# Optimization experiments

Hardware: AMD Instinct MI355X
Metric: run time of the kernel (lower is better)

The kernel has to match this reference:

```python
import jax, jax.numpy as jnp
import numpy as np

DIM = 1024
INNER = DIM // 2
DSTATE = 8
KSZ = 3
DTRANK = max(INNER // 8, 4)
B, L = 4, 4096


def setup_inputs() -> dict:
    key = jax.random.key(0)
    ks = jax.random.split(key, 8)
    s = 0.02
    x = jax.random.normal(ks[0], (B, L, DIM), dtype=jnp.float32)
    W_in = jax.random.normal(ks[1], (DIM, DIM), dtype=jnp.float32) * s
    Kx = jax.random.normal(ks[2], (INNER, 1, KSZ), dtype=jnp.float32) * 0.1
    Kz = jax.random.normal(ks[3], (INNER, 1, KSZ), dtype=jnp.float32) * 0.1
    W_xproj = jax.random.normal(ks[4], (DTRANK + 2 * DSTATE, INNER), dtype=jnp.float32) * s
    W_dt = jax.random.normal(ks[5], (INNER, DTRANK), dtype=jnp.float32) * s
    # dt bias: inverse_softplus of exp(linspace(log dt_min, log dt_max))
    dt_init = jnp.exp(jnp.linspace(jnp.log(0.02), jnp.log(0.2), INNER))
    b_dt = jnp.log(jnp.expm1(dt_init)).astype(jnp.float32)
    A_log = jnp.log(jnp.tile(jnp.arange(1, DSTATE + 1, dtype=jnp.float32), (INNER, 1)))
    D = jnp.ones((INNER,), dtype=jnp.float32)
    W_out = jax.random.normal(ks[6], (DIM, DIM), dtype=jnp.float32) * s
    return {"x": x, "W_in": W_in, "Kx": Kx, "Kz": Kz, "W_xproj": W_xproj,
            "W_dt": W_dt, "b_dt": b_dt, "A_log": A_log, "D": D, "W_out": W_out}


def _dwconv_silu(u, kern):
    # u: [B,L,C], kern: [C,1,K] depthwise (groups=C), 'same' padding
    c = u.shape[-1]
    v = jnp.transpose(u, (0, 2, 1))  # [B,C,L]
    v = jax.lax.conv_general_dilated(v, kern, (1,), [(KSZ // 2, KSZ // 2)],
                                     dimension_numbers=("NCH", "OIH", "NCH"),
                                     feature_group_count=c)
    return jax.nn.silu(jnp.transpose(v, (0, 2, 1)))


def _forward(x, W_in, Kx, Kz, W_xproj, W_dt, b_dt, A_log, D, W_out):
    h = jnp.einsum("bld,ed->ble", x, W_in)  # Linear(dim,dim), no bias
    xb, zb = jnp.split(h, 2, axis=-1)       # [B,L,INNER] each
    xb = _dwconv_silu(xb, Kx)
    zb = _dwconv_silu(zb, Kz)
    proj = jnp.einsum("blc,oc->blo", xb, W_xproj)
    dt_raw = proj[..., :DTRANK]
    b_raw = proj[..., DTRANK:DTRANK + DSTATE]
    c_raw = proj[..., DTRANK + DSTATE:]
    delta = jnp.clip(jax.nn.softplus(jnp.einsum("blr,cr->blc", dt_raw, W_dt) + b_dt), 1e-4, 1.0)  # [B,L,C]
    b_term = jnp.tanh(b_raw)  # [B,L,N]
    c_term = jnp.tanh(c_raw)  # [B,L,N]
    a = jax.nn.softplus(A_log) + 1e-4  # [C,N]
    decay = jnp.clip(jnp.exp(-delta[..., None] * a), 1e-4, 1.0)        # [B,L,C,N]
    drive = (1.0 - decay) * (b_term[:, :, None, :] * xb[..., None])    # [B,L,C,N]

    def step(state, inp):
        dec_t, drv_t, c_t, x_t = inp  # [B,C,N], [B,C,N], [B,N], [B,C]
        state = dec_t * state + drv_t
        y = jnp.sum(state * c_t[:, None, :], axis=-1) + D * x_t  # [B,C]
        return state, y

    tm = lambda t: jnp.moveaxis(t, 1, 0)  # time-major
    state0 = jnp.zeros((x.shape[0], INNER, DSTATE), dtype=jnp.float32)
    _, ys = jax.lax.scan(step, state0, (tm(decay), tm(drive), tm(c_term), tm(xb)))
    y = jnp.moveaxis(ys, 0, 1)  # [B,L,INNER]
    return jnp.einsum("bld,ed->ble", jnp.concatenate([y, zb], axis=-1), W_out)


def reference(x, W_in, Kx, Kz, W_xproj, W_dt, b_dt, A_log, D, W_out):
    return _forward(x, W_in, Kx, Kz, W_xproj, W_dt, b_dt, A_log, D, W_out)
```

## Files before the change

kernel.cpp:

```cpp
#include <hip/hip_runtime.h>


using bf16x8 = __attribute__((ext_vector_type(8))) short;
using f32x4  = __attribute__((ext_vector_type(4))) float;

__device__ __forceinline__ unsigned short f2bf(float f) {
  unsigned int u = __float_as_uint(f);
  u = u + 0x7fffu + ((u >> 16) & 1u);
  return (unsigned short)(u >> 16);
}

__device__ __forceinline__ float fsoftplus(float x) {
  return (x > 15.f) ? x : __logf(1.f + __expf(x));
}

__device__ __forceinline__ float ftanh(float x) {
  float v = fminf(fmaxf(x, -15.f), 15.f);
  float e = __expf(2.f * v);
  return (e - 1.f) / (e + 1.f);
}

__device__ __forceinline__ void cvt4(const float* __restrict__ in,
                                     unsigned short* __restrict__ out, int i) {
  float4 v = ((const float4*)in)[i];
  ushort4 o;
  o.x = f2bf(v.x); o.y = f2bf(v.y); o.z = f2bf(v.z); o.w = f2bf(v.w);
  ((ushort4*)out)[i] = o;
}

__global__ __launch_bounds__(256) void prep_all(
    const float* __restrict__ x, const float* __restrict__ Win,
    const float* __restrict__ Wout, const float* __restrict__ Wdt,
    const float* __restrict__ Wxp,
    unsigned short* __restrict__ xbf, unsigned short* __restrict__ winbf,
    unsigned short* __restrict__ woutbf, unsigned short* __restrict__ wdbf,
    unsigned short* __restrict__ wxpbf) {
  int b = blockIdx.x, t = threadIdx.x;
  if (b < 16384)      cvt4(x,    xbf,    b * 256 + t);
  else if (b < 17408) cvt4(Win,  winbf,  (b - 16384) * 256 + t);
  else if (b < 18432) cvt4(Wout, woutbf, (b - 17408) * 256 + t);
  else if (b < 18464) cvt4(Wdt,  wdbf,   (b - 18432) * 256 + t);
  else {
    int i = (b - 18464) * 256 + t;
    int row = i >> 9;
    wxpbf[i] = (row < 80) ? f2bf(Wxp[i]) : (unsigned short)0;
  }
}


__global__ __launch_bounds__(256) void gemm_proj128(
    const unsigned short* __restrict__ A,
    const unsigned short* __restrict__ B,
    unsigned short* __restrict__ dtr, float* __restrict__ bterm,
    float* __restrict__ cterm, int M, int N, int K) {
  __shared__ short As[128 * 32];
  __shared__ short Bs[128 * 32];
  const int m0 = blockIdx.x * 128;
  const int lane = threadIdx.x & 63;
  const int wv = threadIdx.x >> 6;
  const int wm = (wv >> 1) * 64;
  const int wn = (wv & 1) * 64;
  f32x4 acc[4][4] = {};
  const int row_a = wv * 32 + (lane >> 2);
  const int koff = (lane & 3) * 8;
  const unsigned short* gA = A + (size_t)(m0 + row_a) * K + koff;
  const unsigned short* gB = B + (size_t)row_a * K + koff;
  short* lA = &As[(wv * 32) * 32];
  short* lB = &Bs[(wv * 32) * 32];
  const int r = lane & 15;
  const int q = lane >> 4;
  for (int k0 = 0; k0 < K; k0 += 32) {
    __syncthreads();
    __builtin_amdgcn_global_load_lds((const __attribute__((address_space(1))) void*)(const void*)gA,
                                     (__attribute__((address_space(3))) void*)(void*)lA, 16, 0, 0);
    __builtin_amdgcn_global_load_lds((const __attribute__((address_space(1))) void*)(const void*)(gA + 16 * K),
                                     (__attribute__((address_space(3))) void*)(void*)(lA + 16 * 32), 16, 0, 0);
    __builtin_amdgcn_global_load_lds((const __attribute__((address_space(1))) void*)(const void*)gB,
                                     (__attribute__((address_space(3))) void*)(void*)lB, 16, 0, 0);
    __builtin_amdgcn_global_load_lds((const __attribute__((address_space(1))) void*)(const void*)(gB + 16 * K),
                                     (__attribute__((address_space(3))) void*)(void*)(lB + 16 * 32), 16, 0, 0);
    gA += 32; gB += 32;
    __syncthreads();
    bf16x8 av[4], bv[4];
#pragma unroll
    for (int i = 0; i < 4; ++i)
      av[i] = *(const bf16x8*)&As[(wm + i * 16 + r) * 32 + q * 8];
#pragma unroll
    for (int j = 0; j < 4; ++j)
      bv[j] = *(const bf16x8*)&Bs[(wn + j * 16 + r) * 32 + q * 8];
#pragma unroll
    for (int i = 0; i < 4; ++i)
#pragma unroll
      for (int j = 0; j < 4; ++j)
        acc[i][j] = __builtin_amdgcn_mfma_f32_16x16x32_bf16(av[i], bv[j], acc[i][j], 0, 0, 0);
  }
#pragma unroll
  for (int i = 0; i < 4; ++i)
#pragma unroll
    for (int j = 0; j < 4; ++j) {
      const int col = wn + j * 16 + r;
#pragma unroll
      for (int t = 0; t < 4; ++t) {
        const int row = m0 + wm + i * 16 + q * 4 + t;
        float v = acc[i][j][t];
        if (col < 64)      dtr[(size_t)row * 64 + col] = f2bf(v);
        else if (col < 72) bterm[(size_t)row * 8 + (col - 64)] = ftanh(v);
        else if (col < 80) cterm[(size_t)row * 8 + (col - 72)] = ftanh(v);
      }
    }
}

__global__ __launch_bounds__(256) void gemm_dt128(
    const unsigned short* __restrict__ A,
    const unsigned short* __restrict__ B,
    const float* __restrict__ bdt,
    float* __restrict__ C, int M, int N, int K) {
  __shared__ short As[128 * 32];
  __shared__ short Bs[128 * 32];
  const int m0 = blockIdx.x * 128;
  const int n0 = blockIdx.y * 128;
  const int lane = threadIdx.x & 63;
  const int wv = threadIdx.x >> 6;
  const int wm = (wv >> 1) * 64;
  const int wn = (wv & 1) * 64;
  f32x4 acc[4][4] = {};
  const int row_a = wv * 32 + (lane >> 2);
  const int koff = (lane & 3) * 8;
  const unsigned short* gA = A + (size_t)(m0 + row_a) * K + koff;
  const unsigned short* gB = B + (size_t)(n0 + row_a) * K + koff;
  short* lA = &As[(wv * 32) * 32];
  short* lB = &Bs[(wv * 32) * 32];
  const int r = lane & 15;
  const int q = lane >> 4;
  for (int k0 = 0; k0 < K; k0 += 32) {
    __syncthreads();
    __builtin_amdgcn_global_load_lds((const __attribute__((address_space(1))) void*)(const void*)gA,
                                     (__attribute__((address_space(3))) void*)(void*)lA, 16, 0, 0);
    __builtin_amdgcn_global_load_lds((const __attribute__((address_space(1))) void*)(const void*)(gA + 16 * K),
                                     (__attribute__((address_space(3))) void*)(void*)(lA + 16 * 32), 16, 0, 0);
    __builtin_amdgcn_global_load_lds((const __attribute__((address_space(1))) void*)(const void*)gB,
                                     (__attribute__((address_space(3))) void*)(void*)lB, 16, 0, 0);
    __builtin_amdgcn_global_load_lds((const __attribute__((address_space(1))) void*)(const void*)(gB + 16 * K),
                                     (__attribute__((address_space(3))) void*)(void*)(lB + 16 * 32), 16, 0, 0);
    gA += 32; gB += 32;
    __syncthreads();
    bf16x8 av[4], bv[4];
#pragma unroll
    for (int i = 0; i < 4; ++i)
      av[i] = *(const bf16x8*)&As[(wm + i * 16 + r) * 32 + q * 8];
#pragma unroll
    for (int j = 0; j < 4; ++j)
      bv[j] = *(const bf16x8*)&Bs[(wn + j * 16 + r) * 32 + q * 8];
#pragma unroll
    for (int i = 0; i < 4; ++i)
#pragma unroll
      for (int j = 0; j < 4; ++j)
        acc[i][j] = __builtin_amdgcn_mfma_f32_16x16x32_bf16(av[i], bv[j], acc[i][j], 0, 0, 0);
  }
#pragma unroll
  for (int j = 0; j < 4; ++j) {
    const int col = n0 + wn + j * 16 + r;
    const float bb = bdt[col];
#pragma unroll
    for (int i = 0; i < 4; ++i)
#pragma unroll
      for (int t = 0; t < 4; ++t) {
        float v = acc[i][j][t] + bb;
        float delta = fminf(fmaxf(fsoftplus(v), 1e-4f), 1.f);
        C[(size_t)(m0 + wm + i * 16 + q * 4 + t) * N + col] = delta;
      }
  }
}

__device__ __forceinline__ void g256_stage(short* lds, int slot,
    const unsigned short* sp, int ktIdx, int wvLds, int K) {
  const unsigned short* s = sp + ktIdx * 64;
  __builtin_amdgcn_global_load_lds((const __attribute__((address_space(1))) void*)s,
      (__attribute__((address_space(3))) void*)(lds + slot * 8192 + wvLds), 16, 0, 0);
  __builtin_amdgcn_global_load_lds((const __attribute__((address_space(1))) void*)(s + (size_t)64 * K),
      (__attribute__((address_space(3))) void*)(lds + slot * 8192 + 4096 + wvLds), 16, 0, 0);
}

template <int PAR, int MH, int NHLO, bool RA, bool RB, int SSLOT, bool VM, bool HINT>
__device__ __forceinline__ void g256_phase(
    short* lds, int aSlotOff, int bSlotOff, int aoff, int boff, int wvLds,
    bf16x8 (&av)[4][2], bf16x8 (&bv)[4][2], f32x4 (&acc)[8][4],
    const unsigned short* sp, int ktIdx, int K) {
  if (RA) {
#pragma unroll
    for (int ii = 0; ii < 4; ++ii) {
      av[ii][0] = *(const bf16x8*)&lds[PAR * 4 * 8192 + aSlotOff + MH * 4096 + ii * 1024 + aoff];
      av[ii][1] = *(const bf16x8*)&lds[PAR * 4 * 8192 + aSlotOff + MH * 4096 + ii * 1024 + (aoff ^ 32)];
    }
  }
  if (RB) {
#pragma unroll
    for (int jj = 0; jj < 2; ++jj) {
      bv[NHLO + jj][0] = *(const bf16x8*)&lds[(PAR * 4 + 2) * 8192 + bSlotOff + (NHLO + jj) * 1024 + boff];
      bv[NHLO + jj][1] = *(const bf16x8*)&lds[(PAR * 4 + 2) * 8192 + bSlotOff + (NHLO + jj) * 1024 + (boff ^ 32)];
    }
  }
  g256_stage(lds, SSLOT, sp, ktIdx, wvLds, K);
  if (HINT) asm volatile("s_waitcnt lgkmcnt(8)");
  if (VM) asm volatile("s_waitcnt vmcnt(4)" ::: "memory");
  __builtin_amdgcn_s_barrier();
  asm volatile("s_waitcnt lgkmcnt(0)" ::: "memory");
  __builtin_amdgcn_s_setprio(1);
#pragma unroll
  for (int ii = 0; ii < 4; ++ii)
#pragma unroll
    for (int jj = 0; jj < 2; ++jj) {
      acc[MH * 4 + ii][NHLO + jj] = __builtin_amdgcn_mfma_f32_16x16x32_bf16(
          av[ii][0], bv[NHLO + jj][0], acc[MH * 4 + ii][NHLO + jj], 0, 0, 0);
      acc[MH * 4 + ii][NHLO + jj] = __builtin_amdgcn_mfma_f32_16x16x32_bf16(
          av[ii][1], bv[NHLO + jj][1], acc[MH * 4 + ii][NHLO + jj], 0, 0, 0);
    }
  __builtin_amdgcn_s_setprio(0);
  __builtin_amdgcn_s_barrier();
}

__global__ __launch_bounds__(512, 2) void gemm256_bt(
    const unsigned short* __restrict__ A,
    const unsigned short* __restrict__ B,
    float* __restrict__ C, int M, int N, int K) {
  __shared__ short lds[8 * 8192];
  const int nmt = M >> 8;
  const int bid = blockIdx.x;
  const int g = nmt >> 3;
  const int xcd = bid & 7;
  const int loc = bid >> 3;
  const int mtile = xcd * g + (loc % g);
  const int ntile = loc / g;
  const int m0 = mtile << 8, n0 = ntile << 8;
  const int tid = threadIdx.x;
  const int w = tid >> 6, lane = tid & 63;
  const int r = lane & 15, q = lane >> 4;
  const int wrow = w >> 2, wcol = w & 3;
  const int srow = tid >> 3;
  const int scol = ((tid & 7) ^ (srow & 7)) << 3;
  const unsigned short* pA0 = A + (size_t)(m0 + srow) * K + scol;
  const unsigned short* pA1 = A + (size_t)(m0 + 128 + srow) * K + scol;
  const unsigned short* pB0 = B + (size_t)(n0 + srow) * K + scol;
  const unsigned short* pB1 = B + (size_t)(n0 + 128 + srow) * K + scol;
  const int wvLds = w * 512;
  const int aSlotOff = wrow * 8192;
  const int bSlotOff = (wcol >> 1) * 8192;
  const int swzc = (q * 8) ^ ((r & 7) << 3);
  const int aoff = r * 64 + swzc;
  const int boff = (wcol & 1) * 4096 + r * 64 + swzc;
  bf16x8 av[4][2], bv[4][2];
  f32x4 acc[8][4] = {};
  const int NT = K >> 6;
  const int NI = NT >> 1;
  g256_stage(lds, 0, pA0, 0, wvLds, K);
  g256_stage(lds, 1, pA1, 0, wvLds, K);
  g256_stage(lds, 2, pB0, 0, wvLds, K);
  g256_stage(lds, 3, pB1, 0, wvLds, K);
  g256_stage(lds, 6, pB0, 1, wvLds, K);
  g256_stage(lds, 7, pB1, 1, wvLds, K);
  asm volatile("s_waitcnt vmcnt(4)" ::: "memory");
  __builtin_amdgcn_s_barrier();
#pragma unroll 1
  for (int it = 0; it < NI; ++it) {
    const int ktO  = 2 * it + 1;
    const int ktE2 = (2 * it + 2 < NT) ? 2 * it + 2 : NT - 1;
    const int ktO2 = (2 * it + 3 < NT) ? 2 * it + 3 : NT - 1;
    g256_phase<0, 0, 0, true,  true,  4, false, true >(lds, aSlotOff, bSlotOff, aoff, boff, wvLds, av, bv, acc, pA0, ktO,  K);
    g256_phase<0, 0, 2, false, true,  5, false, false>(lds, aSlotOff, bSlotOff, aoff, boff, wvLds, av, bv, acc, pA1, ktO,  K);
    g256_phase<0, 1, 2, true,  false, 2, false, false>(lds, aSlotOff, bSlotOff, aoff, boff, wvLds, av, bv, acc, pB0, ktE2, K);
    g256_phase<0, 1, 0, false, false, 0, true,  false>(lds, aSlotOff, bSlotOff, aoff, boff, wvLds, av, bv, acc, pA0, ktE2, K);
    g256_phase<1, 0, 0, true,  true,  1, false, true >(lds, aSlotOff, bSlotOff, aoff, boff, wvLds, av, bv, acc, pA1, ktE2, K);
    g256_phase<1, 0, 2, false, true,  3, false, false>(lds, aSlotOff, bSlotOff, aoff, boff, wvLds, av, bv, acc, pB1, ktE2, K);
    g256_phase<1, 1, 2, true,  false, 6, false, false>(lds, aSlotOff, bSlotOff, aoff, boff, wvLds, av, bv, acc, pB0, ktO2, K);
    g256_phase<1, 1, 0, false, false, 7, true,  false>(lds, aSlotOff, bSlotOff, aoff, boff, wvLds, av, bv, acc, pB1, ktO2, K);
  }
  asm volatile("s_waitcnt vmcnt(0) lgkmcnt(0)" ::: "memory");
  float* Cw = C + (size_t)(m0 + wrow * 128) * N + n0 + wcol * 64;
#pragma unroll
  for (int ii = 0; ii < 8; ++ii)
#pragma unroll
    for (int jj = 0; jj < 4; ++jj)
#pragma unroll
      for (int t = 0; t < 4; ++t)
        Cw[(size_t)(ii * 16 + q * 4 + t) * N + jj * 16 + r] = acc[ii][jj][t];
}

__global__ __launch_bounds__(256) void conv_silu_roll(
    const float* __restrict__ h, const float* __restrict__ Kx, const float* __restrict__ Kz,
    float* __restrict__ xb, unsigned short* __restrict__ xbbf,
    unsigned short* __restrict__ cat) {
  const int c4 = threadIdx.x << 2;
  const int bt = blockIdx.x >> 8;
  const int lt = blockIdx.x & 255;
  const int l0 = lt << 4;
  const float* Kp; int c;
  if (c4 < 512) { Kp = Kx; c = c4; } else { Kp = Kz; c = c4 - 512; }
  const float4* K4 = (const float4*)(Kp + c * 3);
  const float4 ka = K4[0], kb = K4[1], kc = K4[2];
  size_t rowbase = ((size_t)bt * 4096 + l0) * 1024 + c4;
  size_t xrow    = ((size_t)bt * 4096 + l0) * 512 + c4;
  const float4 zero = make_float4(0.f, 0.f, 0.f, 0.f);
  float4 um = (l0 > 0) ? *(const float4*)(h + rowbase - 1024) : zero;
  float4 u0 = *(const float4*)(h + rowbase);
#pragma unroll 4
  for (int s = 0; s < 16; ++s) {
    const int l = l0 + s;
    float4 up = (l < 4095) ? *(const float4*)(h + rowbase + 1024) : zero;
    float v0 = um.x * ka.x + u0.x * ka.y + up.x * ka.z;
    float v1 = um.y * ka.w + u0.y * kb.x + up.y * kb.y;
    float v2 = um.z * kb.z + u0.z * kb.w + up.z * kc.x;
    float v3 = um.w * kc.y + u0.w * kc.z + up.w * kc.w;
    float o0 = v0 / (1.f + __expf(-v0));
    float o1 = v1 / (1.f + __expf(-v1));
    float o2 = v2 / (1.f + __expf(-v2));
    float o3 = v3 / (1.f + __expf(-v3));
    ushort4 ob;
    ob.x = f2bf(o0); ob.y = f2bf(o1); ob.z = f2bf(o2); ob.w = f2bf(o3);
    if (c4 < 512) {
      *(float4*)(xb + xrow) = make_float4(o0, o1, o2, o3);
      *(ushort4*)(xbbf + xrow) = ob;
    } else {
      *(ushort4*)(cat + rowbase) = ob;
    }
    um = u0; u0 = up;
    rowbase += 1024; xrow += 512;
  }
}

__global__ __launch_bounds__(256) void scan_p1(
    const float* __restrict__ delta_in, const float* __restrict__ bterm,
    const float* __restrict__ xb, const float* __restrict__ A_log,
    float* __restrict__ Aprod, float* __restrict__ Bpart) {
  int tid = threadIdx.x;
  int gid = blockIdx.x;
  int chunk = gid & 127, half = (gid >> 7) & 1, b = gid >> 8;
  int c = half * 256 + tid;
  float4 a0 = *(const float4*)&A_log[c * 8];
  float4 a1 = *(const float4*)&A_log[c * 8 + 4];
  float na[8] = {a0.x, a0.y, a0.z, a0.w, a1.x, a1.y, a1.z, a1.w};
#pragma unroll
  for (int s = 0; s < 8; ++s) na[s] = -(fsoftplus(na[s]) + 1e-4f);
  int l0 = chunk * 32;
  size_t base  = ((size_t)b * 4096 + l0) * 512 + c;
  size_t bbase = ((size_t)b * 4096 + l0) * 8;
  float S[8] = {}, Ap[8] = {1.f, 1.f, 1.f, 1.f, 1.f, 1.f, 1.f, 1.f};
  for (int i = 0; i < 32; ++i) {
    float delta = delta_in[base];
    float xv = xb[base];
    float4 bt0 = *(const float4*)&bterm[bbase];
    float4 bt1 = *(const float4*)&bterm[bbase + 4];
    float bt[8] = {bt0.x, bt0.y, bt0.z, bt0.w, bt1.x, bt1.y, bt1.z, bt1.w};
#pragma unroll
    for (int s = 0; s < 8; ++s) {
      float dec = fminf(fmaxf(__expf(delta * na[s]), 1e-4f), 1.f);
      float btx = bt[s] * xv;
      S[s] = dec * S[s] + (btx - dec * btx);
      Ap[s] *= dec;
    }
    base += 512; bbase += 8;
  }
  size_t o = (size_t)chunk * 16384 + ((size_t)(b * 512 + c)) * 8;
  *(float4*)&Aprod[o]     = make_float4(Ap[0], Ap[1], Ap[2], Ap[3]);
  *(float4*)&Aprod[o + 4] = make_float4(Ap[4], Ap[5], Ap[6], Ap[7]);
  *(float4*)&Bpart[o]     = make_float4(S[0], S[1], S[2], S[3]);
  *(float4*)&Bpart[o + 4] = make_float4(S[4], S[5], S[6], S[7]);
}

__global__ __launch_bounds__(64) void scan_p2(
    const float* __restrict__ Aprod, const float* __restrict__ Bpart,
    float* __restrict__ initst) {
  int t = blockIdx.x * 64 + threadIdx.x;
  float st = 0.f;
  for (int cb = 0; cb < 128; cb += 8) {
    float a[8], bb[8];
#pragma unroll
    for (int j = 0; j < 8; ++j) {
      size_t o = (size_t)(cb + j) * 16384 + t;
      a[j] = Aprod[o]; bb[j] = Bpart[o];
    }
#pragma unroll
    for (int j = 0; j < 8; ++j) {
      size_t o = (size_t)(cb + j) * 16384 + t;
      initst[o] = st;
      st = a[j] * st + bb[j];
    }
  }
}

__global__ __launch_bounds__(256) void scan_p3(
    const float* __restrict__ delta_in, const float* __restrict__ bterm,
    const float* __restrict__ cterm, const float* __restrict__ xb,
    const float* __restrict__ A_log, const float* __restrict__ Dp,
    const float* __restrict__ initst, unsigned short* __restrict__ cat) {
  int tid = threadIdx.x;
  int gid = blockIdx.x;
  int chunk = gid & 127, half = (gid >> 7) & 1, b = gid >> 8;
  int c = half * 256 + tid;
  float4 a0 = *(const float4*)&A_log[c * 8];
  float4 a1 = *(const float4*)&A_log[c * 8 + 4];
  float na[8] = {a0.x, a0.y, a0.z, a0.w, a1.x, a1.y, a1.z, a1.w};
#pragma unroll
  for (int s = 0; s < 8; ++s) na[s] = -(fsoftplus(na[s]) + 1e-4f);
  float Dv = Dp[c];
  size_t o = (size_t)chunk * 16384 + ((size_t)(b * 512 + c)) * 8;
  float4 s0 = *(const float4*)&initst[o];
  float4 s1 = *(const float4*)&initst[o + 4];
  float S[8] = {s0.x, s0.y, s0.z, s0.w, s1.x, s1.y, s1.z, s1.w};
  int l0 = chunk * 32;
  size_t base  = ((size_t)b * 4096 + l0) * 512 + c;
  size_t bbase = ((size_t)b * 4096 + l0) * 8;
  size_t cbase = ((size_t)b * 4096 + l0) * 1024 + c;
  for (int i = 0; i < 32; ++i) {
    float delta = delta_in[base];
    float xv = xb[base];
    float4 bt0 = *(const float4*)&bterm[bbase];
    float4 bt1 = *(const float4*)&bterm[bbase + 4];
    float4 ct0 = *(const float4*)&cterm[bbase];
    float4 ct1 = *(const float4*)&cterm[bbase + 4];
    float bt[8] = {bt0.x, bt0.y, bt0.z, bt0.w, bt1.x, bt1.y, bt1.z, bt1.w};
    float ct[8] = {ct0.x, ct0.y, ct0.z, ct0.w, ct1.x, ct1.y, ct1.z, ct1.w};
    float acc = Dv * xv;
#pragma unroll
    for (int s = 0; s < 8; ++s) {
      float dec = fminf(fmaxf(__expf(delta * na[s]), 1e-4f), 1.f);
      float btx = bt[s] * xv;
      S[s] = dec * S[s] + (btx - dec * btx);
      acc += S[s] * ct[s];
    }
    cat[cbase] = f2bf(acc);
    base += 512; bbase += 8; cbase += 1024;
  }
}

extern "C" void kernel_launch(void* const* d_in, const int* in_sizes, int n_in,
                              void* d_out, int out_size, void* d_ws, size_t ws_size,
                              hipStream_t stream) {
  (void)in_sizes; (void)n_in; (void)out_size; (void)ws_size;
  const float* x       = (const float*)d_in[0];
  const float* W_in    = (const float*)d_in[1];
  const float* Kx      = (const float*)d_in[2];
  const float* Kz      = (const float*)d_in[3];
  const float* W_xproj = (const float*)d_in[4];
  const float* W_dt    = (const float*)d_in[5];
  const float* b_dt    = (const float*)d_in[6];
  const float* A_log   = (const float*)d_in[7];
  const float* Dp      = (const float*)d_in[8];
  const float* W_out   = (const float*)d_in[9];
  float* out = (float*)d_out;

  char* w = (char*)d_ws;
  unsigned short* xbf  = (unsigned short*)(w);
  float* xb    = (float*)(w + 33554432);
  float* draw  = (float*)(w + 67108864);
  float* bterm = (float*)(w + 100663296);
  float* cterm = (float*)(w + 101187584);
  float* Aprod = (float*)(w + 101711872);
  float* Bpart = (float*)(w + 110100480);
  float* initst = (float*)(w + 118489088);
  unsigned short* winbf  = (unsigned short*)(w + 126877696);
  unsigned short* woutbf = (unsigned short*)(w + 128974848);
  unsigned short* dtr    = (unsigned short*)(w + 131072000);
  unsigned short* wxp_bf = (unsigned short*)(w + 133169152);
  unsigned short* wd_bf  = (unsigned short*)(w + 133300224);
  unsigned short* xbbf = (unsigned short*)Aprod;
  float* h = out;

  prep_all<<<18720, 256, 0, stream>>>(x, W_in, W_out, W_dt, W_xproj,
                                      xbf, winbf, woutbf, wd_bf, wxp_bf);

  gemm256_bt<<<256, 512, 0, stream>>>(xbf, winbf, h, 16384, 1024, 1024);

  conv_silu_roll<<<1024, 256, 0, stream>>>(h, Kx, Kz, xb, xbbf, xbf );

  gemm_proj128<<<128, 256, 0, stream>>>(xbbf, wxp_bf, dtr, bterm, cterm, 16384, 128, 512);
  gemm_dt128<<<dim3(128, 4), 256, 0, stream>>>(dtr, wd_bf, b_dt, draw, 16384, 512, 64);

  scan_p1<<<1024, 256, 0, stream>>>(draw, bterm, xb, A_log, Aprod, Bpart);
  scan_p2<<<256, 64, 0, stream>>>(Aprod, Bpart, initst);
  scan_p3<<<1024, 256, 0, stream>>>(draw, bterm, cterm, xb, A_log, Dp, initst, xbf );

  gemm256_bt<<<256, 512, 0, stream>>>(xbf, woutbf, out, 16384, 1024, 1024);
}
```

Measured before the change: 312.1 us.

## Fuse scan phase-1 chunk reduction into delta projection GEMM epilogue

Merges the scan_p1 kernel into the epilogue of the dt GEMM. Each block stages its computed delta tile in LDS in two 64-row passes and runs the per-chunk decay and drive reduction straight from shared memory. This removes one kernel launch and the global re-read of delta in phase 1, though delta is still written out for phase 3. In exchange the GEMM block does extra serial scan work with only 128 channel threads active per pass, adds barriers, and raises LDS use to about 33 KB.

Result: slower. 319.7 us (+2.5%).

```diff
diff --git a/kernel.cpp b/kernel.cpp
--- a/kernel.cpp
+++ b/kernel.cpp
@@ -110,13 +110,18 @@
     }
 }
 
-__global__ __launch_bounds__(256) void gemm_dt128(
+__global__ __launch_bounds__(256, 4) void gemm_dt_scan1(
     const unsigned short* __restrict__ A,
     const unsigned short* __restrict__ B,
     const float* __restrict__ bdt,
-    float* __restrict__ C, int M, int N, int K) {
-  __shared__ short As[128 * 32];
-  __shared__ short Bs[128 * 32];
+    const float* __restrict__ xb, const float* __restrict__ bterm,
+    const float* __restrict__ A_log,
+    float* __restrict__ draw,
+    float* __restrict__ Aprod, float* __restrict__ Bpart,
+    int M, int N, int K) {
+  __shared__ float arena[64 * 129];
+  short* As = (short*)arena;
+  short* Bs = (short*)arena + 4096;
   const int m0 = blockIdx.x * 128;
   const int n0 = blockIdx.y * 128;
   const int lane = threadIdx.x & 63;
@@ -157,18 +162,72 @@
       for (int j = 0; j < 4; ++j)
         acc[i][j] = __builtin_amdgcn_mfma_f32_16x16x32_bf16(av[i], bv[j], acc[i][j], 0, 0, 0);
   }
-#pragma unroll
-  for (int j = 0; j < 4; ++j) {
-    const int col = n0 + wn + j * 16 + r;
-    const float bb = bdt[col];
-#pragma unroll
-    for (int i = 0; i < 4; ++i)
-#pragma unroll
-      for (int t = 0; t < 4; ++t) {
-        float v = acc[i][j][t] + bb;
-        float delta = fminf(fmaxf(fsoftplus(v), 1e-4f), 1.f);
-        C[(size_t)(m0 + wm + i * 16 + q * 4 + t) * N + col] = delta;
+  float bb4[4];
+#pragma unroll
+  for (int j = 0; j < 4; ++j) bb4[j] = bdt[n0 + wn + j * 16 + r];
+  const int cl = threadIdx.x & 127;
+  const int cg = n0 + cl;
+  const int b  = m0 >> 12;
+  const int l0 = m0 & 4095;
+  float na[8];
+  {
+    float4 a0 = *(const float4*)&A_log[cg * 8];
+    float4 a1 = *(const float4*)&A_log[cg * 8 + 4];
+    na[0] = a0.x; na[1] = a0.y; na[2] = a0.z; na[3] = a0.w;
+    na[4] = a1.x; na[5] = a1.y; na[6] = a1.z; na[7] = a1.w;
+#pragma unroll
+    for (int s = 0; s < 8; ++s) na[s] = -(fsoftplus(na[s]) + 1e-4f);
+  }
+  float (*dl)[129] = (float(*)[129])arena;
+  __syncthreads();
+#pragma unroll 1
+  for (int pass = 0; pass < 2; ++pass) {
+    if ((wv >> 1) == pass) {
+#pragma unroll
+      for (int j = 0; j < 4; ++j) {
+        const int col = wn + j * 16 + r;
+#pragma unroll
+        for (int i = 0; i < 4; ++i)
+#pragma unroll
+          for (int t = 0; t < 4; ++t) {
+            const int rl = i * 16 + q * 4 + t;
+            float v = acc[i][j][t] + bb4[j];
+            float delta = fminf(fmaxf(fsoftplus(v), 1e-4f), 1.f);
+            draw[(size_t)(m0 + pass * 64 + rl) * N + n0 + col] = delta;
+            dl[rl][col] = delta;
+          }
       }
+    }
+    __syncthreads();
+    {
+      const int chl = (pass << 1) + (threadIdx.x >> 7);
+      const int chunk = (l0 >> 5) + chl;
+      const int lr0 = (chl & 1) * 32;
+      size_t xbase = ((size_t)b * 4096 + l0 + chl * 32) * 512 + cg;
+      size_t bbase = ((size_t)b * 4096 + l0 + chl * 32) * 8;
+      float S[8] = {}, Ap[8] = {1.f, 1.f, 1.f, 1.f, 1.f, 1.f, 1.f, 1.f};
+      for (int i = 0; i < 32; ++i) {
+        float delta = dl[lr0 + i][cl];
+        float xv = xb[xbase];
+        float4 bt0 = *(const float4*)&bterm[bbase];
+        float4 bt1 = *(const float4*)&bterm[bbase + 4];
+        float bt[8] = {bt0.x, bt0.y, bt0.z, bt0.w, bt1.x, bt1.y, bt1.z, bt1.w};
+#pragma unroll
+        for (int s = 0; s < 8; ++s) {
+          float dec = fminf(fmaxf(__expf(delta * na[s]), 1e-4f), 1.f);
+          float btx = bt[s] * xv;
+          S[s] = dec * S[s] + (btx - dec * btx);
+          Ap[s] *= dec;
+        }
+        xbase += 512; bbase += 8;
+      }
+      size_t o = (size_t)chunk * 16384 + ((size_t)(b * 512 + cg)) * 8;
+      *(float4*)&Aprod[o]     = make_float4(Ap[0], Ap[1], Ap[2], Ap[3]);
+      *(float4*)&Aprod[o + 4] = make_float4(Ap[4], Ap[5], Ap[6], Ap[7]);
+      *(float4*)&Bpart[o]     = make_float4(S[0], S[1], S[2], S[3]);
+      *(float4*)&Bpart[o + 4] = make_float4(S[4], S[5], S[6], S[7]);
+    }
+    __syncthreads();
   }
 }
 
@@ -327,45 +386,6 @@
   }
 }
 
-__global__ __launch_bounds__(256) void scan_p1(
-    const float* __restrict__ delta_in, const float* __restrict__ bterm,
-    const float* __restrict__ xb, const float* __restrict__ A_log,
-    float* __restrict__ Aprod, float* __restrict__ Bpart) {
-  int tid = threadIdx.x;
-  int gid = blockIdx.x;
-  int chunk = gid & 127, half = (gid >> 7) & 1, b = gid >> 8;
-  int c = half * 256 + tid;
-  float4 a0 = *(const float4*)&A_log[c * 8];
-  float4 a1 = *(const float4*)&A_log[c * 8 + 4];
-  float na[8] = {a0.x, a0.y, a0.z, a0.w, a1.x, a1.y, a1.z, a1.w};
-#pragma unroll
-  for (int s = 0; s < 8; ++s) na[s] = -(fsoftplus(na[s]) + 1e-4f);
-  int l0 = chunk * 32;
-  size_t base  = ((size_t)b * 4096 + l0) * 512 + c;
-  size_t bbase = ((size_t)b * 4096 + l0) * 8;
-  float S[8] = {}, Ap[8] = {1.f, 1.f, 1.f, 1.f, 1.f, 1.f, 1.f, 1.f};
-  for (int i = 0; i < 32; ++i) {
-    float delta = delta_in[base];
-    float xv = xb[base];
-    float4 bt0 = *(const float4*)&bterm[bbase];
-    float4 bt1 = *(const float4*)&bterm[bbase + 4];
-    float bt[8] = {bt0.x, bt0.y, bt0.z, bt0.w, bt1.x, bt1.y, bt1.z, bt1.w};
-#pragma unroll
-    for (int s = 0; s < 8; ++s) {
-      float dec = fminf(fmaxf(__expf(delta * na[s]), 1e-4f), 1.f);
-      float btx = bt[s] * xv;
-      S[s] = dec * S[s] + (btx - dec * btx);
-      Ap[s] *= dec;
-    }
-    base += 512; bbase += 8;
-  }
-  size_t o = (size_t)chunk * 16384 + ((size_t)(b * 512 + c)) * 8;
-  *(float4*)&Aprod[o]     = make_float4(Ap[0], Ap[1], Ap[2], Ap[3]);
-  *(float4*)&Aprod[o + 4] = make_float4(Ap[4], Ap[5], Ap[6], Ap[7]);
-  *(float4*)&Bpart[o]     = make_float4(S[0], S[1], S[2], S[3]);
-  *(float4*)&Bpart[o + 4] = make_float4(S[4], S[5], S[6], S[7]);
-}
-
 __global__ __launch_bounds__(64) void scan_p2(
     const float* __restrict__ Aprod, const float* __restrict__ Bpart,
     float* __restrict__ initst) {
@@ -473,9 +493,9 @@
   conv_silu_roll<<<1024, 256, 0, stream>>>(h, Kx, Kz, xb, xbbf, xbf );
 
   gemm_proj128<<<128, 256, 0, stream>>>(xbbf, wxp_bf, dtr, bterm, cterm, 16384, 128, 512);
-  gemm_dt128<<<dim3(128, 4), 256, 0, stream>>>(dtr, wd_bf, b_dt, draw, 16384, 512, 64);
-
-  scan_p1<<<1024, 256, 0, stream>>>(draw, bterm, xb, A_log, Aprod, Bpart);
+  gemm_dt_scan1<<<dim3(128, 4), 256, 0, stream>>>(
+      dtr, wd_bf, b_dt, xb, bterm, A_log, draw, Aprod, Bpart, 16384, 512, 64);
+
   scan_p2<<<256, 64, 0, stream>>>(Aprod, Bpart, initst);
   scan_p3<<<1024, 256, 0, stream>>>(draw, bterm, cterm, xb, A_log, Dp, initst, xbf );
 
```
